# Optimization experiments

Hardware: AMD Instinct MI355X
Metric: run time of the kernel (lower is better)

## Reference

```python
import jax, jax.numpy as jnp
import numpy as np

NUM_TOKENS = 2048
HIDDEN = 2048
INTERM = 768
NUM_EXPERTS = 16
TOP_K = 8


def setup_inputs() -> dict:
    key = jax.random.key(0)
    k1, k2, k3, k4, k5 = jax.random.split(key, 5)
    hidden_states = jax.random.normal(k1, (NUM_TOKENS, HIDDEN), dtype=jnp.float32)
    # scale weights ~N(0, 0.02) like typical transformer init to keep activations sane
    gate_up_proj = jax.random.normal(k2, (NUM_EXPERTS, HIDDEN, 2 * INTERM), dtype=jnp.float32) * 0.02
    down_proj = jax.random.normal(k3, (NUM_EXPERTS, INTERM, HIDDEN), dtype=jnp.float32) * 0.02
    expert_indices = jax.random.randint(k4, (NUM_TOKENS, TOP_K), 0, NUM_EXPERTS, dtype=jnp.int32)
    expert_weights = jax.random.uniform(k5, (NUM_TOKENS, TOP_K), dtype=jnp.float32)
    return {
        "hidden_states": hidden_states,
        "gate_up_proj": gate_up_proj,
        "down_proj": down_proj,
        "expert_indices": expert_indices,
        "expert_weights": expert_weights,
    }


def reference(hidden_states, gate_up_proj, down_proj, expert_indices, expert_weights):
    T, H = hidden_states.shape
    E, _, I2 = gate_up_proj.shape
    I = I2 // 2
    # Dense dispatch over the (small, fixed) expert axis -- same math as the
    # per-token top-k fallback, vectorized. gate_up: [T, E, 2I]
    gate_up = jnp.einsum("th,ehi->tei", hidden_states, gate_up_proj)
    gate, up = gate_up[..., :I], gate_up[..., I:]
    activated = jax.nn.silu(gate) * up                      # [T, E, I]
    expert_out = jnp.einsum("tei,eih->teh", activated, down_proj)  # [T, E, H]
    # Per-token routing weights scattered onto the dense expert axis: [T, E]
    combine = jnp.zeros((T, E), dtype=hidden_states.dtype)
    combine = combine.at[jnp.arange(T)[:, None], expert_indices].add(expert_weights)
    output = jnp.einsum("te,teh->th", combine, expert_out)  # [T, H]
    return output
```

## Files before the change

### kernel.cpp

```cpp
#include <hip/hip_runtime.h>
#include <hip/hip_bf16.h>

#define T_TOK 2048
#define HID 2048
#define IMED 768
#define NEXP 16
#define TOPK 8
#define MAXPAIR (T_TOK * TOPK)

using f32x4  = __attribute__((ext_vector_type(4))) float;
using bf16x8 = __attribute__((ext_vector_type(8))) __bf16;

__device__ __forceinline__ f32x4 mfma16(bf16x8 a, bf16x8 b, f32x4 c) {
  return __builtin_amdgcn_mfma_f32_16x16x32_bf16(a, b, c, 0, 0, 0);
}

__device__ __forceinline__ void gload16(const void* g, void* lds) {
  __builtin_amdgcn_global_load_lds((const __attribute__((address_space(1))) unsigned int*)g,
                                   (__attribute__((address_space(3))) unsigned int*)lds,
                                   16, 0, 0);
}

__global__ void moe_cvt_x(const float* __restrict__ X, __bf16* __restrict__ XB) {
  int i = (blockIdx.x * blockDim.x + threadIdx.x) * 8;
  float4 v0 = *(const float4*)&X[i];
  float4 v1 = *(const float4*)&X[i + 4];
  bf16x8 o;
  o[0] = (__bf16)v0.x; o[1] = (__bf16)v0.y; o[2] = (__bf16)v0.z; o[3] = (__bf16)v0.w;
  o[4] = (__bf16)v1.x; o[5] = (__bf16)v1.y; o[6] = (__bf16)v1.z; o[7] = (__bf16)v1.w;
  *(bf16x8*)&XB[i] = o;
}

__global__ __launch_bounds__(256) void moe_transpose(const float* __restrict__ in,
                                                     __bf16* __restrict__ out,
                                                     int R, int C) {
  __shared__ __align__(16) float tile[64][68];
  const int e = blockIdx.z;
  const float* ib = in + (size_t)e * R * C;
  __bf16* ob = out + (size_t)e * R * C;
  const int c0 = blockIdx.x * 64, r0 = blockIdx.y * 64;
  const int tid = threadIdx.x;
  const int lr = tid >> 4;
  const int lc = (tid & 15) * 4;
#pragma unroll
  for (int i = 0; i < 4; ++i) {
    int r = lr + i * 16;
    float4 v = *(const float4*)&ib[(size_t)(r0 + r) * C + c0 + lc];
    *(float4*)&tile[r][lc] = v;
  }
  __syncthreads();
  const int oc = tid >> 2;
  const int sr = (tid & 3) * 16;
  bf16x8 o0, o1;
#pragma unroll
  for (int j = 0; j < 8; ++j) o0[j] = (__bf16)tile[sr + j][oc];
#pragma unroll
  for (int j = 0; j < 8; ++j) o1[j] = (__bf16)tile[sr + 8 + j][oc];
  *(bf16x8*)&ob[(size_t)(c0 + oc) * R + r0 + sr] = o0;
  *(bf16x8*)&ob[(size_t)(c0 + oc) * R + r0 + sr + 8] = o1;
}

__global__ void moe_route_build(const int* __restrict__ idx, const float* __restrict__ wgt,
                                float* __restrict__ combine, int* __restrict__ meta) {
  int t = blockIdx.x * blockDim.x + threadIdx.x;
  if (t >= T_TOK) return;
  float c[NEXP];
#pragma unroll
  for (int e = 0; e < NEXP; ++e) c[e] = 0.f;
  for (int k = 0; k < TOPK; ++k) c[idx[t * TOPK + k]] += wgt[t * TOPK + k];
  for (int e = 0; e < NEXP; ++e) {
    combine[t * NEXP + e] = c[e];
    if (c[e] != 0.f) atomicAdd(&meta[e], 1);
  }
}

__global__ void moe_scan(int* __restrict__ meta) {
  if (threadIdx.x == 0 && blockIdx.x == 0) {
    int s = 0;
    for (int e = 0; e < NEXP; ++e) { meta[16 + e] = s; meta[33 + e] = s; s += meta[e]; }
    meta[32] = s;
  }
}

__global__ void moe_scatter(const float* __restrict__ combine, int* __restrict__ meta,
                            int* __restrict__ route_tok, float* __restrict__ route_w,
                            int* __restrict__ ptok, int* __restrict__ pcnt) {
  int t = blockIdx.x * blockDim.x + threadIdx.x;
  if (t >= T_TOK) return;
  int slot = 0;
  for (int e = 0; e < NEXP; ++e) {
    float c = combine[t * NEXP + e];
    if (c != 0.f) {
      int p = atomicAdd(&meta[33 + e], 1);
      route_tok[p] = t;
      route_w[p] = c;
      ptok[t * TOPK + slot] = p;
      ++slot;
    }
  }
  pcnt[t] = slot;
}

__global__ __launch_bounds__(256) void moe_gemm1(
    const __bf16* __restrict__ XB, const __bf16* __restrict__ WguT,
    const int* __restrict__ rtok, const float* __restrict__ rw,
    const int* __restrict__ meta, __bf16* __restrict__ ACT) {
  const int orig = blockIdx.x;
  const int wgid = (orig & 7) * 384 + (orig >> 3);
  const int mx = wgid & 15;
  const int ny = (wgid >> 4) % 12;
  const int e  = wgid / 192;

  const int seg0 = meta[16 + e];
  const int cnt  = meta[16 + e + 1] - seg0;
  const int m0 = mx * 128;
  if (m0 >= cnt) return;
  const int n0 = ny * 64;

  __shared__ char As[16384];
  __shared__ char Bs[16384];

  const int tid = threadIdx.x;
  const int l = tid & 63;
  const int w = tid >> 6;
  const int wm = w >> 1, wn = w & 1;
  const int swoff = 16 * ((l & 7) ^ (l >> 3));

  const char* baseA[4];
  const char* baseB[4];
#pragma unroll
  for (int q = 0; q < 4; ++q) {
    const int r = (w * 4 + q) * 8 + (l >> 3);
    int grow = m0 + r; if (grow >= cnt) grow = cnt - 1;
    const int tok = rtok[seg0 + grow];
    baseA[q] = (const char*)(XB + (size_t)tok * HID) + swoff;
    const int sec = r >> 6, s = r & 63;
    const int wrow = (s < 32) ? (n0 + sec * 32 + s) : (IMED + n0 + sec * 32 + (s - 32));
    baseB[q] = (const char*)(WguT + ((size_t)e * (2 * IMED) + wrow) * HID) + swoff;
  }

  f32x4 acc[4][4];
  const f32x4 zero = {0.f, 0.f, 0.f, 0.f};
#pragma unroll
  for (int i = 0; i < 4; ++i)
#pragma unroll
    for (int j = 0; j < 4; ++j) acc[i][j] = zero;

  for (int k0b = 0; k0b < HID * 2; k0b += 128) {
#pragma unroll
    for (int q = 0; q < 4; ++q) {
      gload16(baseA[q] + k0b, &As[(w * 4 + q) * 1024]);
      gload16(baseB[q] + k0b, &Bs[(w * 4 + q) * 1024]);
    }
    __syncthreads();
#pragma unroll
    for (int ks = 0; ks < 2; ++ks) {
      const int colb = ks * 64 + (l >> 4) * 16;
      bf16x8 af[4], bf[4];
#pragma unroll
      for (int mi = 0; mi < 4; ++mi) {
        const int row = wm * 64 + mi * 16 + (l & 15);
        af[mi] = *(const bf16x8*)&As[row * 128 + (colb ^ ((row & 7) << 4))];
      }
#pragma unroll
      for (int ni = 0; ni < 4; ++ni) {
        const int row = wn * 64 + ni * 16 + (l & 15);
        bf[ni] = *(const bf16x8*)&Bs[row * 128 + (colb ^ ((row & 7) << 4))];
      }
#pragma unroll
      for (int mi = 0; mi < 4; ++mi)
#pragma unroll
        for (int ni = 0; ni < 4; ++ni)
          acc[mi][ni] = mfma16(af[mi], bf[ni], acc[mi][ni]);
    }
    __syncthreads();
  }

  const int cbase = n0 + wn * 32;
#pragma unroll
  for (int mi = 0; mi < 4; ++mi) {
    const int rb = wm * 64 + mi * 16 + ((l >> 4) << 2);
#pragma unroll
    for (int r = 0; r < 4; ++r) {
      const int row = m0 + rb + r;
      if (row < cnt) {
        const float wgt = rw[seg0 + row];
#pragma unroll
        for (int ni = 0; ni < 2; ++ni) {
          const float g = acc[mi][ni][r];
          const float u = acc[mi][ni + 2][r];
          const float s = g / (1.f + __expf(-g));
          ACT[(size_t)(seg0 + row) * IMED + cbase + ni * 16 + (l & 15)] = (__bf16)(s * u * wgt);
        }
      }
    }
  }
}

__global__ __launch_bounds__(256) void moe_gemm2(
    const __bf16* __restrict__ ACT, const __bf16* __restrict__ WdT,
    const int* __restrict__ meta, __bf16* __restrict__ ACT2) {
  const int orig = blockIdx.x;
  const int wgid = (orig & 7) * 512 + (orig >> 3);
  const int mx = wgid & 15;
  const int ny = (wgid >> 4) & 15;
  const int e  = wgid >> 8;

  const int seg0 = meta[16 + e];
  const int cnt  = meta[16 + e + 1] - seg0;
  const int m0 = mx * 128;
  if (m0 >= cnt) return;
  const int n0 = ny * 128;

  __shared__ char As[16384];
  __shared__ char Bs[16384];

  const int tid = threadIdx.x;
  const int l = tid & 63;
  const int w = tid >> 6;
  const int wm = w >> 1, wn = w & 1;
  const int swoff = 16 * ((l & 7) ^ (l >> 3));

  const char* baseA[4];
  const char* baseB[4];
#pragma unroll
  for (int q = 0; q < 4; ++q) {
    const int r = (w * 4 + q) * 8 + (l >> 3);
    int grow = m0 + r; if (grow >= cnt) grow = cnt - 1;
    baseA[q] = (const char*)(ACT + (size_t)(seg0 + grow) * IMED) + swoff;
    baseB[q] = (const char*)(WdT + ((size_t)e * HID + n0 + r) * IMED) + swoff;
  }

  f32x4 acc[4][4];
  const f32x4 zero = {0.f, 0.f, 0.f, 0.f};
#pragma unroll
  for (int i = 0; i < 4; ++i)
#pragma unroll
    for (int j = 0; j < 4; ++j) acc[i][j] = zero;

  for (int k0b = 0; k0b < IMED * 2; k0b += 128) {
#pragma unroll
    for (int q = 0; q < 4; ++q) {
      gload16(baseA[q] + k0b, &As[(w * 4 + q) * 1024]);
      gload16(baseB[q] + k0b, &Bs[(w * 4 + q) * 1024]);
    }
    __syncthreads();
#pragma unroll
    for (int ks = 0; ks < 2; ++ks) {
      const int colb = ks * 64 + (l >> 4) * 16;
      bf16x8 af[4], bf[4];
#pragma unroll
      for (int mi = 0; mi < 4; ++mi) {
        const int row = wm * 64 + mi * 16 + (l & 15);
        af[mi] = *(const bf16x8*)&As[row * 128 + (colb ^ ((row & 7) << 4))];
      }
#pragma unroll
      for (int ni = 0; ni < 4; ++ni) {
        const int row = wn * 64 + ni * 16 + (l & 15);
        bf[ni] = *(const bf16x8*)&Bs[row * 128 + (colb ^ ((row & 7) << 4))];
      }
#pragma unroll
      for (int mi = 0; mi < 4; ++mi)
#pragma unroll
        for (int ni = 0; ni < 4; ++ni)
          acc[mi][ni] = mfma16(af[mi], bf[ni], acc[mi][ni]);
    }
    __syncthreads();
  }

#pragma unroll
  for (int mi = 0; mi < 4; ++mi) {
    const int rb = wm * 64 + mi * 16 + ((l >> 4) << 2);
#pragma unroll
    for (int r = 0; r < 4; ++r) {
      const int row = m0 + rb + r;
      if (row < cnt) {
#pragma unroll
        for (int ni = 0; ni < 4; ++ni)
          ACT2[(size_t)(seg0 + row) * HID + n0 + wn * 64 + ni * 16 + (l & 15)] =
              (__bf16)acc[mi][ni][r];
      }
    }
  }
}

__global__ __launch_bounds__(256) void moe_combine(const __bf16* __restrict__ ACT2,
                                                   const int* __restrict__ ptok,
                                                   const int* __restrict__ pcnt,
                                                   float* __restrict__ out) {
  const int t = blockIdx.x;
  const int h = threadIdx.x * 8;
  const int n = pcnt[t];
  float a[8];
#pragma unroll
  for (int j = 0; j < 8; ++j) a[j] = 0.f;
  for (int k = 0; k < n; ++k) {
    const int p = ptok[t * TOPK + k];
    bf16x8 v = *(const bf16x8*)&ACT2[(size_t)p * HID + h];
#pragma unroll
    for (int j = 0; j < 8; ++j) a[j] += (float)v[j];
  }
  float4 o0 = {a[0], a[1], a[2], a[3]};
  float4 o1 = {a[4], a[5], a[6], a[7]};
  *(float4*)&out[(size_t)t * HID + h] = o0;
  *(float4*)&out[(size_t)t * HID + h + 4] = o1;
}

extern "C" void kernel_launch(void* const* d_in, const int* in_sizes, int n_in,
                              void* d_out, int out_size, void* d_ws, size_t ws_size,
                              hipStream_t stream) {
  const float* X   = (const float*)d_in[0];
  const float* GUP = (const float*)d_in[1];
  const float* DP  = (const float*)d_in[2];
  const int*   IDX = (const int*)d_in[3];
  const float* W   = (const float*)d_in[4];
  float* out = (float*)d_out;

  size_t off = 0;
  auto alloc = [&](size_t bytes) -> void* {
    void* p = (char*)d_ws + off;
    off = (off + bytes + 255) & ~(size_t)255;
    return p;
  };
  __bf16* XB      = (__bf16*)alloc((size_t)T_TOK * HID * 2);
  __bf16* WguT    = (__bf16*)alloc((size_t)NEXP * 2 * IMED * HID * 2);
  __bf16* WdT     = (__bf16*)alloc((size_t)NEXP * HID * IMED * 2);
  __bf16* ACT     = (__bf16*)alloc((size_t)(MAXPAIR + 128) * IMED * 2);
  float*  combine = (float*)alloc((size_t)T_TOK * NEXP * 4);
  int*    meta    = (int*)alloc(64 * 4);
  int*    rtok    = (int*)alloc((size_t)MAXPAIR * 4);
  float*  rw      = (float*)alloc((size_t)MAXPAIR * 4);
  int*    ptok    = (int*)alloc((size_t)T_TOK * TOPK * 4);
  int*    pcnt    = (int*)alloc((size_t)T_TOK * 4);
  if (off > ws_size) return;

  __bf16* ACT2 = WguT;

  hipMemsetAsync(meta, 0, 256, stream);
  moe_cvt_x<<<T_TOK * HID / (256 * 8), 256, 0, stream>>>(X, XB);
  moe_transpose<<<dim3((2 * IMED) / 64, HID / 64, NEXP), 256, 0, stream>>>(GUP, WguT, HID, 2 * IMED);
  moe_transpose<<<dim3(HID / 64, IMED / 64, NEXP), 256, 0, stream>>>(DP, WdT, IMED, HID);
  moe_route_build<<<T_TOK / 256, 256, 0, stream>>>(IDX, W, combine, meta);
  moe_scan<<<1, 64, 0, stream>>>(meta);
  moe_scatter<<<T_TOK / 256, 256, 0, stream>>>(combine, meta, rtok, rw, ptok, pcnt);
  moe_gemm1<<<3072, 256, 0, stream>>>(XB, WguT, rtok, rw, meta, ACT);
  moe_gemm2<<<4096, 256, 0, stream>>>(ACT, WdT, meta, ACT2);
  moe_combine<<<T_TOK, 256, 0, stream>>>(ACT2, ptok, pcnt, out);
}
```

Before: 325.9 us.

## Enlarge gemm1 tiles to 256x128 with 4-stage async LDS pipeline

The gate/up grouped GEMM now uses 512-thread blocks computing 256x128 output tiles with a K step of 32. A four-slot LDS ring buffer is fed by direct global-to-LDS loads issued three steps ahead, with explicit vmcnt/lgkmcnt waits, barriers and raised MFMA priority so loads overlap compute. This removes the per-iteration full sync stall of the old single-buffered loop and raises data reuse per block. The cost is 128KB of LDS, larger register use, fewer blocks, and more padding waste on partially filled expert segments.

```diff
diff --git a/kernel.cpp b/kernel.cpp
--- a/kernel.cpp
+++ b/kernel.cpp
@@ -20,6 +20,13 @@
                                    (__attribute__((address_space(3))) unsigned int*)lds,
                                    16, 0, 0);
 }
+
+#define BAR() do { asm volatile("s_barrier" ::: "memory"); \
+                   __builtin_amdgcn_sched_barrier(0); } while (0)
+#define LGKM0() do { asm volatile("s_waitcnt lgkmcnt(0)" ::: "memory"); \
+                     __builtin_amdgcn_sched_barrier(0); } while (0)
+#define WAITV(N) do { asm volatile("s_waitcnt vmcnt(" #N ")" ::: "memory"); \
+                      __builtin_amdgcn_sched_barrier(0); } while (0)
 
 __global__ void moe_cvt_x(const float* __restrict__ X, __bf16* __restrict__ XB) {
   int i = (blockIdx.x * blockDim.x + threadIdx.x) * 8;
@@ -101,85 +108,111 @@
   pcnt[t] = slot;
 }
 
-__global__ __launch_bounds__(256) void moe_gemm1(
+__global__ __launch_bounds__(512, 2) void moe_gemm1(
     const __bf16* __restrict__ XB, const __bf16* __restrict__ WguT,
     const int* __restrict__ rtok, const float* __restrict__ rw,
     const int* __restrict__ meta, __bf16* __restrict__ ACT) {
   const int orig = blockIdx.x;
-  const int wgid = (orig & 7) * 384 + (orig >> 3);
-  const int mx = wgid & 15;
-  const int ny = (wgid >> 4) % 12;
-  const int e  = wgid / 192;
+  const int wgid = (orig & 7) * 96 + (orig >> 3);
+  const int e   = wgid / 48;
+  const int rem = wgid % 48;
+  const int ny  = rem >> 3;
+  const int mx  = rem & 7;
 
   const int seg0 = meta[16 + e];
   const int cnt  = meta[16 + e + 1] - seg0;
-  const int m0 = mx * 128;
+  const int m0 = mx * 256;
   if (m0 >= cnt) return;
-  const int n0 = ny * 64;
-
-  __shared__ char As[16384];
-  __shared__ char Bs[16384];
+  const int n0 = ny * 128;
+
+  __shared__ __align__(16) char As[4 * 16384];
+  __shared__ __align__(16) char Bs[4 * 16384];
 
   const int tid = threadIdx.x;
   const int l = tid & 63;
   const int w = tid >> 6;
-  const int wm = w >> 1, wn = w & 1;
-  const int swoff = 16 * ((l & 7) ^ (l >> 3));
-
-  const char* baseA[4];
-  const char* baseB[4];
-#pragma unroll
-  for (int q = 0; q < 4; ++q) {
-    const int r = (w * 4 + q) * 8 + (l >> 3);
-    int grow = m0 + r; if (grow >= cnt) grow = cnt - 1;
+  const int wm = w >> 2, wn = w & 3;
+
+  const char* baseA[2];
+  const char* baseB[2];
+#pragma unroll
+  for (int q = 0; q < 2; ++q) {
+    const int row = (w * 2 + q) * 16 + (l >> 2);
+    const int g   = (l & 3) ^ ((row >> 1) & 3);
+    int grow = m0 + row; if (grow >= cnt) grow = cnt - 1;
     const int tok = rtok[seg0 + grow];
-    baseA[q] = (const char*)(XB + (size_t)tok * HID) + swoff;
-    const int sec = r >> 6, s = r & 63;
-    const int wrow = (s < 32) ? (n0 + sec * 32 + s) : (IMED + n0 + sec * 32 + (s - 32));
-    baseB[q] = (const char*)(WguT + ((size_t)e * (2 * IMED) + wrow) * HID) + swoff;
-  }
-
-  f32x4 acc[4][4];
+    baseA[q] = (const char*)(XB + (size_t)tok * HID) + g * 16;
+    const int sec = row >> 6, s = row & 63;
+    const int wr = (s < 32) ? (n0 + sec * 32 + s) : (IMED + n0 + sec * 32 + (s - 32));
+    baseB[q] = (const char*)(WguT + ((size_t)e * (2 * IMED) + wr) * HID) + g * 16;
+  }
+
+  f32x4 acc[8][4];
   const f32x4 zero = {0.f, 0.f, 0.f, 0.f};
 #pragma unroll
-  for (int i = 0; i < 4; ++i)
+  for (int i = 0; i < 8; ++i)
 #pragma unroll
     for (int j = 0; j < 4; ++j) acc[i][j] = zero;
 
-  for (int k0b = 0; k0b < HID * 2; k0b += 128) {
-#pragma unroll
-    for (int q = 0; q < 4; ++q) {
-      gload16(baseA[q] + k0b, &As[(w * 4 + q) * 1024]);
-      gload16(baseB[q] + k0b, &Bs[(w * 4 + q) * 1024]);
-    }
-    __syncthreads();
-#pragma unroll
-    for (int ks = 0; ks < 2; ++ks) {
-      const int colb = ks * 64 + (l >> 4) * 16;
-      bf16x8 af[4], bf[4];
-#pragma unroll
-      for (int mi = 0; mi < 4; ++mi) {
-        const int row = wm * 64 + mi * 16 + (l & 15);
-        af[mi] = *(const bf16x8*)&As[row * 128 + (colb ^ ((row & 7) << 4))];
-      }
-#pragma unroll
-      for (int ni = 0; ni < 4; ++ni) {
-        const int row = wn * 64 + ni * 16 + (l & 15);
-        bf[ni] = *(const bf16x8*)&Bs[row * 128 + (colb ^ ((row & 7) << 4))];
-      }
-#pragma unroll
-      for (int mi = 0; mi < 4; ++mi)
-#pragma unroll
-        for (int ni = 0; ni < 4; ++ni)
-          acc[mi][ni] = mfma16(af[mi], bf[ni], acc[mi][ni]);
-    }
-    __syncthreads();
+  auto STAGE_A = [&](int slot, int t) {
+#pragma unroll
+    for (int q = 0; q < 2; ++q)
+      gload16(baseA[q] + t * 64, &As[slot * 16384 + (w * 2 + q) * 1024]);
+  };
+  auto STAGE_B = [&](int slot, int t) {
+#pragma unroll
+    for (int q = 0; q < 2; ++q)
+      gload16(baseB[q] + t * 64, &Bs[slot * 16384 + (w * 2 + q) * 1024]);
+  };
+
+  const int rdbase = (l & 15) * 64 + (((l >> 4) ^ ((l >> 1) & 3)) * 16);
+
+  const int NT = HID / 32;
+  STAGE_A(0, 0); STAGE_B(0, 0);
+  STAGE_A(1, 1); STAGE_B(1, 1);
+  STAGE_A(2, 2); STAGE_B(2, 2);
+  WAITV(8); BAR();
+
+#pragma unroll 1
+  for (int t = 0; t < NT; ++t) {
+    const char* Ab = &As[(t & 3) * 16384] + wm * 8192 + rdbase;
+    const char* Bb = &Bs[(t & 3) * 16384] + wn * 4096 + rdbase;
+    bf16x8 af[4], bf[4];
+#pragma unroll
+    for (int mi = 0; mi < 4; ++mi) af[mi] = *(const bf16x8*)(Ab + mi * 1024);
+#pragma unroll
+    for (int ni = 0; ni < 4; ++ni) bf[ni] = *(const bf16x8*)(Bb + ni * 1024);
+    if (t + 3 < NT) STAGE_A((t + 3) & 3, t + 3);
+    BAR(); LGKM0();
+    __builtin_amdgcn_s_setprio(1);
+#pragma unroll
+    for (int mi = 0; mi < 4; ++mi)
+#pragma unroll
+      for (int ni = 0; ni < 4; ++ni)
+        acc[mi][ni] = mfma16(af[mi], bf[ni], acc[mi][ni]);
+    __builtin_amdgcn_s_setprio(0);
+    BAR();
+#pragma unroll
+    for (int mi = 0; mi < 4; ++mi) af[mi] = *(const bf16x8*)(Ab + (4 + mi) * 1024);
+    if (t + 3 < NT) STAGE_B((t + 3) & 3, t + 3);
+    BAR(); LGKM0();
+    __builtin_amdgcn_s_setprio(1);
+#pragma unroll
+    for (int mi = 0; mi < 4; ++mi)
+#pragma unroll
+      for (int ni = 0; ni < 4; ++ni)
+        acc[4 + mi][ni] = mfma16(af[mi], bf[ni], acc[4 + mi][ni]);
+    __builtin_amdgcn_s_setprio(0);
+    if (t + 3 < NT)      { WAITV(8); }
+    else if (t + 2 < NT) { WAITV(4); }
+    else if (t + 1 < NT) { WAITV(0); }
+    BAR();
   }
 
   const int cbase = n0 + wn * 32;
 #pragma unroll
-  for (int mi = 0; mi < 4; ++mi) {
-    const int rb = wm * 64 + mi * 16 + ((l >> 4) << 2);
+  for (int mi = 0; mi < 8; ++mi) {
+    const int rb = wm * 128 + mi * 16 + ((l >> 4) << 2);
 #pragma unroll
     for (int r = 0; r < 4; ++r) {
       const int row = m0 + rb + r;
@@ -325,7 +358,7 @@
   __bf16* XB      = (__bf16*)alloc((size_t)T_TOK * HID * 2);
   __bf16* WguT    = (__bf16*)alloc((size_t)NEXP * 2 * IMED * HID * 2);
   __bf16* WdT     = (__bf16*)alloc((size_t)NEXP * HID * IMED * 2);
-  __bf16* ACT     = (__bf16*)alloc((size_t)(MAXPAIR + 128) * IMED * 2);
+  __bf16* ACT     = (__bf16*)alloc((size_t)(MAXPAIR + 256) * IMED * 2);
   float*  combine = (float*)alloc((size_t)T_TOK * NEXP * 4);
   int*    meta    = (int*)alloc(64 * 4);
   int*    rtok    = (int*)alloc((size_t)MAXPAIR * 4);
@@ -343,7 +376,7 @@
   moe_route_build<<<T_TOK / 256, 256, 0, stream>>>(IDX, W, combine, meta);
   moe_scan<<<1, 64, 0, stream>>>(meta);
   moe_scatter<<<T_TOK / 256, 256, 0, stream>>>(combine, meta, rtok, rw, ptok, pcnt);
-  moe_gemm1<<<3072, 256, 0, stream>>>(XB, WguT, rtok, rw, meta, ACT);
+  moe_gemm1<<<768, 512, 0, stream>>>(XB, WguT, rtok, rw, meta, ACT);
   moe_gemm2<<<4096, 256, 0, stream>>>(ACT, WdT, meta, ACT2);
   moe_combine<<<T_TOK, 256, 0, stream>>>(ACT2, ptok, pcnt, out);
 }
```

Result: no change. 330.1 us (+1.3%).

## Fuse routing into one block and compact GEMM grids over live expert tiles

Applied to the files above, without the earlier changes.

Replaces the route_build, scan and scatter kernels and the meta memset with a single 1024-thread block that counts per-expert tokens in shared memory, computes offsets and per-expert tile prefix counts, then scatters. The GEMM grids are resized to cover only the M-tiles actually in use: 144 tiles times N-tiles, with each block finding its expert by a linear search over the tile prefix. This removes kernel launches and many early-exiting empty blocks. In exchange the routing runs on one workgroup, and the 144-tile bound assumes each token uses at most 8 distinct experts, so there are at most 16 partial tiles.

```diff
diff --git a/kernel.cpp b/kernel.cpp
--- a/kernel.cpp
+++ b/kernel.cpp
@@ -60,45 +60,65 @@
   *(bf16x8*)&ob[(size_t)(c0 + oc) * R + r0 + sr + 8] = o1;
 }
 
-__global__ void moe_route_build(const int* __restrict__ idx, const float* __restrict__ wgt,
-                                float* __restrict__ combine, int* __restrict__ meta) {
-  int t = blockIdx.x * blockDim.x + threadIdx.x;
-  if (t >= T_TOK) return;
-  float c[NEXP];
-#pragma unroll
-  for (int e = 0; e < NEXP; ++e) c[e] = 0.f;
-  for (int k = 0; k < TOPK; ++k) c[idx[t * TOPK + k]] += wgt[t * TOPK + k];
+__global__ __launch_bounds__(1024) void moe_route(const int* __restrict__ idx,
+                                                  const float* __restrict__ wgt,
+                                                  int* __restrict__ meta,
+                                                  int* __restrict__ rtok,
+                                                  float* __restrict__ rw,
+                                                  int* __restrict__ ptok,
+                                                  int* __restrict__ pcnt) {
+  __shared__ int cntS[NEXP];
+  __shared__ int curS[NEXP];
+  const int tid = threadIdx.x;
+  if (tid < NEXP) cntS[tid] = 0;
+  __syncthreads();
+
+  const int t0 = tid, t1 = tid + 1024;
+  float c0[NEXP], c1[NEXP];
+#pragma unroll
+  for (int e = 0; e < NEXP; ++e) { c0[e] = 0.f; c1[e] = 0.f; }
+  for (int k = 0; k < TOPK; ++k) {
+    c0[idx[t0 * TOPK + k]] += wgt[t0 * TOPK + k];
+    c1[idx[t1 * TOPK + k]] += wgt[t1 * TOPK + k];
+  }
+  int n0 = 0, n1 = 0;
+#pragma unroll
   for (int e = 0; e < NEXP; ++e) {
-    combine[t * NEXP + e] = c[e];
-    if (c[e] != 0.f) atomicAdd(&meta[e], 1);
-  }
-}
-
-__global__ void moe_scan(int* __restrict__ meta) {
-  if (threadIdx.x == 0 && blockIdx.x == 0) {
-    int s = 0;
-    for (int e = 0; e < NEXP; ++e) { meta[16 + e] = s; meta[33 + e] = s; s += meta[e]; }
+    if (c0[e] != 0.f) { atomicAdd(&cntS[e], 1); ++n0; }
+    if (c1[e] != 0.f) { atomicAdd(&cntS[e], 1); ++n1; }
+  }
+  pcnt[t0] = n0; pcnt[t1] = n1;
+  __syncthreads();
+
+  if (tid == 0) {
+    int s = 0, b = 0;
+    for (int e = 0; e < NEXP; ++e) {
+      meta[e] = cntS[e];
+      meta[16 + e] = s;
+      meta[49 + e] = b;
+      curS[e] = s;
+      s += cntS[e];
+      b += (cntS[e] + 127) >> 7;
+    }
     meta[32] = s;
-  }
-}
-
-__global__ void moe_scatter(const float* __restrict__ combine, int* __restrict__ meta,
-                            int* __restrict__ route_tok, float* __restrict__ route_w,
-                            int* __restrict__ ptok, int* __restrict__ pcnt) {
-  int t = blockIdx.x * blockDim.x + threadIdx.x;
-  if (t >= T_TOK) return;
-  int slot = 0;
+    meta[65] = b;
+  }
+  __syncthreads();
+
+  int s0 = 0, s1 = 0;
+#pragma unroll
   for (int e = 0; e < NEXP; ++e) {
-    float c = combine[t * NEXP + e];
-    if (c != 0.f) {
-      int p = atomicAdd(&meta[33 + e], 1);
-      route_tok[p] = t;
-      route_w[p] = c;
-      ptok[t * TOPK + slot] = p;
-      ++slot;
-    }
-  }
-  pcnt[t] = slot;
+    if (c0[e] != 0.f) {
+      int p = atomicAdd(&curS[e], 1);
+      rtok[p] = t0; rw[p] = c0[e];
+      ptok[t0 * TOPK + s0] = p; ++s0;
+    }
+    if (c1[e] != 0.f) {
+      int p = atomicAdd(&curS[e], 1);
+      rtok[p] = t1; rw[p] = c1[e];
+      ptok[t1 * TOPK + s1] = p; ++s1;
+    }
+  }
 }
 
 __global__ __launch_bounds__(256) void moe_gemm1(
@@ -106,15 +126,18 @@
     const int* __restrict__ rtok, const float* __restrict__ rw,
     const int* __restrict__ meta, __bf16* __restrict__ ACT) {
   const int orig = blockIdx.x;
-  const int wgid = (orig & 7) * 384 + (orig >> 3);
-  const int mx = wgid & 15;
-  const int ny = (wgid >> 4) % 12;
-  const int e  = wgid / 192;
+  const int wgid = (orig & 7) * 216 + (orig >> 3);
+  const int ny = wgid / 144;
+  const int bi = wgid % 144;
+  if (bi >= meta[65]) return;
+  int e = 0;
+#pragma unroll
+  for (int k = 1; k < NEXP; ++k) if (meta[49 + k] <= bi) e = k;
+  const int mx = bi - meta[49 + e];
 
   const int seg0 = meta[16 + e];
   const int cnt  = meta[16 + e + 1] - seg0;
   const int m0 = mx * 128;
-  if (m0 >= cnt) return;
   const int n0 = ny * 64;
 
   __shared__ char As[16384];
@@ -201,15 +224,18 @@
     const __bf16* __restrict__ ACT, const __bf16* __restrict__ WdT,
     const int* __restrict__ meta, __bf16* __restrict__ ACT2) {
   const int orig = blockIdx.x;
-  const int wgid = (orig & 7) * 512 + (orig >> 3);
-  const int mx = wgid & 15;
-  const int ny = (wgid >> 4) & 15;
-  const int e  = wgid >> 8;
+  const int wgid = (orig & 7) * 288 + (orig >> 3);
+  const int ny = wgid / 144;
+  const int bi = wgid % 144;
+  if (bi >= meta[65]) return;
+  int e = 0;
+#pragma unroll
+  for (int k = 1; k < NEXP; ++k) if (meta[49 + k] <= bi) e = k;
+  const int mx = bi - meta[49 + e];
 
   const int seg0 = meta[16 + e];
   const int cnt  = meta[16 + e + 1] - seg0;
   const int m0 = mx * 128;
-  if (m0 >= cnt) return;
   const int n0 = ny * 128;
 
   __shared__ char As[16384];
@@ -326,8 +352,7 @@
   __bf16* WguT    = (__bf16*)alloc((size_t)NEXP * 2 * IMED * HID * 2);
   __bf16* WdT     = (__bf16*)alloc((size_t)NEXP * HID * IMED * 2);
   __bf16* ACT     = (__bf16*)alloc((size_t)(MAXPAIR + 128) * IMED * 2);
-  float*  combine = (float*)alloc((size_t)T_TOK * NEXP * 4);
-  int*    meta    = (int*)alloc(64 * 4);
+  int*    meta    = (int*)alloc(128 * 4);
   int*    rtok    = (int*)alloc((size_t)MAXPAIR * 4);
   float*  rw      = (float*)alloc((size_t)MAXPAIR * 4);
   int*    ptok    = (int*)alloc((size_t)T_TOK * TOPK * 4);
@@ -336,14 +361,11 @@
 
   __bf16* ACT2 = WguT;
 
-  hipMemsetAsync(meta, 0, 256, stream);
   moe_cvt_x<<<T_TOK * HID / (256 * 8), 256, 0, stream>>>(X, XB);
   moe_transpose<<<dim3((2 * IMED) / 64, HID / 64, NEXP), 256, 0, stream>>>(GUP, WguT, HID, 2 * IMED);
   moe_transpose<<<dim3(HID / 64, IMED / 64, NEXP), 256, 0, stream>>>(DP, WdT, IMED, HID);
-  moe_route_build<<<T_TOK / 256, 256, 0, stream>>>(IDX, W, combine, meta);
-  moe_scan<<<1, 64, 0, stream>>>(meta);
-  moe_scatter<<<T_TOK / 256, 256, 0, stream>>>(combine, meta, rtok, rw, ptok, pcnt);
-  moe_gemm1<<<3072, 256, 0, stream>>>(XB, WguT, rtok, rw, meta, ACT);
-  moe_gemm2<<<4096, 256, 0, stream>>>(ACT, WdT, meta, ACT2);
+  moe_route<<<1, 1024, 0, stream>>>(IDX, W, meta, rtok, rw, ptok, pcnt);
+  moe_gemm1<<<1728, 256, 0, stream>>>(XB, WguT, rtok, rw, meta, ACT);
+  moe_gemm2<<<2304, 256, 0, stream>>>(ACT, WdT, meta, ACT2);
   moe_combine<<<T_TOK, 256, 0, stream>>>(ACT2, ptok, pcnt, out);
 }
```

Result: no change. 329.6 us (+1.1%).
